# Optimization experiments

Measured on AMD Instinct MI355X. Metric: run time of the kernel, lower is better.

Reference implementation:

```python
import jax, jax.numpy as jnp
import numpy as np

# Hardcoded dims from the source module
B, T, C, H, HS, L, V = 512, 128, 96, 6, 16, 6, 65
FF = 4 * C
EPS = 1e-5  # torch LayerNorm default


def _ln(x, g, b):
    m = jnp.mean(x, axis=-1, keepdims=True)
    v = jnp.mean(jnp.square(x - m), axis=-1, keepdims=True)
    return (x - m) * jax.lax.rsqrt(v + EPS) * g + b


def setup_inputs() -> dict:
    key = jax.random.key(0)
    ks = jax.random.split(key, 24)
    s = 0.02
    n = lambda k, shape: (jax.random.normal(k, shape, dtype=jnp.float32) * s)
    return {
        "idx": jax.random.randint(ks[0], (B, T), 0, V, dtype=jnp.int32),
        "tok_emb": n(ks[1], (V, C)),
        "pos_emb": n(ks[2], (T, C)),
        # per-layer, per-head Q/K/V (each Head has its own bias-free Linear)
        "Wq": n(ks[3], (L, H, C, HS)),
        "Wk": n(ks[4], (L, H, C, HS)),
        "Wv": n(ks[5], (L, H, C, HS)),
        "Wp": n(ks[6], (L, C, C)),
        "bp": jnp.zeros((L, C), jnp.float32),
        "W1": n(ks[7], (L, C, FF)),
        "b1": jnp.zeros((L, FF), jnp.float32),
        "W2": n(ks[8], (L, FF, C)),
        "b2": jnp.zeros((L, C), jnp.float32),
        "ln1_g": jnp.ones((L, C), jnp.float32),
        "ln1_b": jnp.zeros((L, C), jnp.float32),
        "ln2_g": jnp.ones((L, C), jnp.float32),
        "ln2_b": jnp.zeros((L, C), jnp.float32),
        "lnf_g": jnp.ones((C,), jnp.float32),
        "lnf_b": jnp.zeros((C,), jnp.float32),
        "Wlm": n(ks[9], (C, V)),
        "blm": jnp.zeros((V,), jnp.float32),
    }


def _forward(idx, tok_emb, pos_emb, Wq, Wk, Wv, Wp, bp, W1, b1, W2, b2,
             ln1_g, ln1_b, ln2_g, ln2_b, lnf_g, lnf_b, Wlm, blm):
    x = tok_emb[idx] + pos_emb[None, :, :]  # [B,T,C]
    mask = jnp.tril(jnp.ones((T, T), dtype=bool))
    scale = HS ** -0.5

    def block(x, p):
        wq, wk, wv, wp, pb, w1, bb1, w2, bb2, g1, be1, g2, be2 = p
        h = _ln(x, g1, be1)
        q = jnp.einsum('btc,hcd->bhtd', h, wq)
        k = jnp.einsum('btc,hcd->bhtd', h, wk)
        v = jnp.einsum('btc,hcd->bhtd', h, wv)
        w = jnp.einsum('bhtd,bhsd->bhts', q, k) * scale
        w = jnp.where(mask, w, -jnp.inf)
        a = jax.nn.softmax(w, axis=-1)
        o = jnp.einsum('bhts,bhsd->bhtd', a, v)
        o = o.transpose(0, 2, 1, 3).reshape(x.shape[0], T, C)  # concat heads
        x = x + (o @ wp + pb)
        h = _ln(x, g2, be2)
        x = x + (jax.nn.relu(h @ w1 + bb1) @ w2 + bb2)
        return x, None

    params = (Wq, Wk, Wv, Wp, bp, W1, b1, W2, b2, ln1_g, ln1_b, ln2_g, ln2_b)
    x, _ = jax.lax.scan(block, x, params)
    x = _ln(x, lnf_g, lnf_b)
    return x @ Wlm + blm  # logits [B,T,V]


def reference(idx, tok_emb, pos_emb, Wq, Wk, Wv, Wp, bp, W1, b1, W2, b2,
              ln1_g, ln1_b, ln2_g, ln2_b, lnf_g, lnf_b, Wlm, blm):
    return _forward(idx, tok_emb, pos_emb, Wq, Wk, Wv, Wp, bp, W1, b1, W2, b2,
                    ln1_g, ln1_b, ln2_g, ln2_b, lnf_g, lnf_b, Wlm, blm)
```

## Files before the change

kernel.cpp:

```cpp
#include <hip/hip_runtime.h>
#include <hip/hip_bf16.h>

#define BB  512
#define TT  128
#define CC  96
#define HH  6
#define HSZ 16
#define LL  6
#define FFD 384
#define VV  65
#define BT  (BB * TT)

using short8  = __attribute__((ext_vector_type(8))) short;
using short4v = __attribute__((ext_vector_type(4))) short;
using f32x4   = __attribute__((ext_vector_type(4))) float;
using half4   = __attribute__((ext_vector_type(4))) _Float16;

static __device__ __forceinline__ unsigned short f2bf(float f) {
  union { float f; unsigned u; } v{f};
  unsigned r = (v.u + 0x7fff + ((v.u >> 16) & 1)) >> 16;
  return (unsigned short)r;
}
static __device__ __forceinline__ float b2f(unsigned short h) {
  union { unsigned u; float f; } v{(unsigned)h << 16};
  return v.f;
}

__global__ __launch_bounds__(256) void embed_kernel(
    const int* __restrict__ idx, const float* __restrict__ tok,
    const float* __restrict__ pos, float* __restrict__ x) {
  int gid = blockIdx.x * 256 + threadIdx.x;
  int r = gid / 24, c4 = gid % 24;
  int t = r & (TT - 1);
  int token = idx[r];
  const float4 a = *(const float4*)&tok[token * CC + c4 * 4];
  const float4 p = *(const float4*)&pos[t * CC + c4 * 4];
  float4 o;
  o.x = a.x + p.x; o.y = a.y + p.y; o.z = a.z + p.z; o.w = a.w + p.w;
  *(float4*)&x[(size_t)r * CC + c4 * 4] = o;
}

__global__ __launch_bounds__(256) void pack_w(
    const float* __restrict__ Wq, const float* __restrict__ Wk,
    const float* __restrict__ Wv, const float* __restrict__ Wp,
    const float* __restrict__ W1, const float* __restrict__ W2,
    const float* __restrict__ Wlm, unsigned short* __restrict__ out) {
  int job = blockIdx.y;
  int e = blockIdx.x * 256 + threadIdx.x;
  int K, sz; size_t obase;
  if (job < 6)       { K = 96;  sz = 27648; obase = (size_t)job * 27648; }
  else if (job < 12) { K = 96;  sz = 9216;  obase = 165888 + (size_t)(job - 6) * 9216; }
  else if (job < 18) { K = 96;  sz = 36864; obase = 221184 + (size_t)(job - 12) * 36864; }
  else if (job < 24) { K = 384; sz = 36864; obase = 442368 + (size_t)(job - 18) * 36864; }
  else               { K = 96;  sz = 7680;  obase = 663552; }
  if (e >= sz) return;
  int j = e & 7, lane = (e >> 3) & 63, rest = e >> 9;
  int KS = K / 32;
  int ks = rest % KS, cb = rest / KS;
  int k = ks * 32 + (lane >> 4) * 8 + j;
  int n = cb * 16 + (lane & 15);
  float val = 0.f;
  if (job < 6) {
    int src = n / 96, nn = n % 96;
    const float* W = (src == 0) ? Wq : (src == 1) ? Wk : Wv;
    val = W[((size_t)(job * 6 + (nn >> 4)) * 96 + k) * 16 + (nn & 15)];
  } else if (job < 12) {
    val = Wp[(size_t)(job - 6) * 9216 + k * 96 + n];
  } else if (job < 18) {
    val = W1[(size_t)(job - 12) * 36864 + k * 384 + n];
  } else if (job < 24) {
    val = W2[(size_t)(job - 18) * 36864 + k * 96 + n];
  } else {
    if (n < 65) val = Wlm[k * 65 + n];
  }
  out[obase + e] = f2bf(val);
}

template<int K, int N, int NS, bool BIAS, bool RELU, bool RES, bool OUTBF>
__global__ __launch_bounds__(256) void mfma_gemm(
    const unsigned short* __restrict__ A, const unsigned short* __restrict__ Wpk,
    const float* __restrict__ bias, const float* __restrict__ res, void* __restrict__ out) {
  constexpr int KS = K / 32;
  const int lane = threadIdx.x & 63;
  const int wave = threadIdx.x >> 6;
  const int r0 = blockIdx.x * 64 + wave * 16;
  const int c15 = lane & 15, kg = lane >> 4;
  short8 a[KS];
  const unsigned short* ap = A + (size_t)(r0 + c15) * K + kg * 8;
#pragma unroll
  for (int ks = 0; ks < KS; ++ks) a[ks] = *(const short8*)(ap + ks * 32);
  const short8* wf = (const short8*)Wpk;
#pragma unroll 1
  for (int cb = 0; cb < N / 16; ++cb) {
    f32x4 acc = {0.f, 0.f, 0.f, 0.f};
#pragma unroll
    for (int ks = 0; ks < KS; ++ks) {
      short8 b = wf[(cb * KS + ks) * 64 + lane];
      acc = __builtin_amdgcn_mfma_f32_16x16x32_bf16(a[ks], b, acc, 0, 0, 0);
    }
    int n = cb * 16 + c15;
#pragma unroll
    for (int i = 0; i < 4; ++i) {
      int row = r0 + kg * 4 + i;
      if (NS == N || n < NS) {
        float v = acc[i];
        if (BIAS) v += bias[n];
        if (RELU) v = fmaxf(v, 0.f);
        if (RES)  v += res[(size_t)row * NS + n];
        if (OUTBF) ((unsigned short*)out)[(size_t)row * NS + n] = f2bf(v);
        else       ((float*)out)[(size_t)row * NS + n] = v;
      }
    }
  }
}

template<int N, int NS, bool BIAS, bool RELU, bool OUTBF>
__global__ __launch_bounds__(256) void ln_gemm(
    const float* __restrict__ X, const unsigned short* __restrict__ Wpk,
    const float* __restrict__ gamma, const float* __restrict__ beta,
    const float* __restrict__ bias, void* __restrict__ out) {
  const int lane = threadIdx.x & 63;
  const int wave = threadIdx.x >> 6;
  const int r0 = blockIdx.x * 64 + wave * 16;
  const int c15 = lane & 15, kg = lane >> 4;
  const float* xp = X + (size_t)(r0 + c15) * CC + kg * 8;
  float xv[24];
  float s = 0.f, s2 = 0.f;
#pragma unroll
  for (int ks = 0; ks < 3; ++ks) {
    float4 lo = *(const float4*)(xp + ks * 32);
    float4 hi = *(const float4*)(xp + ks * 32 + 4);
    xv[ks * 8 + 0] = lo.x; xv[ks * 8 + 1] = lo.y; xv[ks * 8 + 2] = lo.z; xv[ks * 8 + 3] = lo.w;
    xv[ks * 8 + 4] = hi.x; xv[ks * 8 + 5] = hi.y; xv[ks * 8 + 6] = hi.z; xv[ks * 8 + 7] = hi.w;
  }
#pragma unroll
  for (int i = 0; i < 24; ++i) { s += xv[i]; s2 += xv[i] * xv[i]; }
  s  += __shfl_xor(s, 16);  s  += __shfl_xor(s, 32);
  s2 += __shfl_xor(s2, 16); s2 += __shfl_xor(s2, 32);
  const float mean = s * (1.f / 96.f);
  const float rs = rsqrtf(s2 * (1.f / 96.f) - mean * mean + 1e-5f);
  short8 a[3];
#pragma unroll
  for (int ks = 0; ks < 3; ++ks) {
    const int kb = ks * 32 + kg * 8;
    float4 glo = *(const float4*)&gamma[kb];
    float4 ghi = *(const float4*)&gamma[kb + 4];
    float4 blo = *(const float4*)&beta[kb];
    float4 bhi = *(const float4*)&beta[kb + 4];
    const float gg[8] = {glo.x, glo.y, glo.z, glo.w, ghi.x, ghi.y, ghi.z, ghi.w};
    const float bb[8] = {blo.x, blo.y, blo.z, blo.w, bhi.x, bhi.y, bhi.z, bhi.w};
#pragma unroll
    for (int j = 0; j < 8; ++j)
      a[ks][j] = (short)f2bf((xv[ks * 8 + j] - mean) * rs * gg[j] + bb[j]);
  }
  const short8* wf = (const short8*)Wpk;
#pragma unroll 1
  for (int cb = 0; cb < N / 16; ++cb) {
    f32x4 acc = {0.f, 0.f, 0.f, 0.f};
#pragma unroll
    for (int ks = 0; ks < 3; ++ks) {
      short8 b = wf[(cb * 3 + ks) * 64 + lane];
      acc = __builtin_amdgcn_mfma_f32_16x16x32_bf16(a[ks], b, acc, 0, 0, 0);
    }
    int n = cb * 16 + c15;
#pragma unroll
    for (int i = 0; i < 4; ++i) {
      int row = r0 + kg * 4 + i;
      if (NS == N || n < NS) {
        float v = acc[i];
        if (BIAS) v += bias[n];
        if (RELU) v = fmaxf(v, 0.f);
        if (OUTBF) ((unsigned short*)out)[(size_t)row * NS + n] = f2bf(v);
        else       ((float*)out)[(size_t)row * NS + n] = v;
      }
    }
  }
}

__global__ __launch_bounds__(256) void attn_mfma(
    const unsigned short* __restrict__ qkv, unsigned short* __restrict__ aout) {
  const int b = blockIdx.x / HH, hd = blockIdx.x % HH;
  __shared__ _Float16 Ks[TT][20];
  __shared__ _Float16 Vs[TT][20];
  const size_t base = (size_t)b * TT * 288 + hd * HSZ;
  const int t = threadIdx.x;
  const int r = t >> 1, part = t & 1;

  {
    const short8 k8 = *(const short8*)&qkv[base + (size_t)r * 288 + 96  + part * 8];
    const short8 v8 = *(const short8*)&qkv[base + (size_t)r * 288 + 192 + part * 8];
    half4 klo, khi, vlo, vhi;
#pragma unroll
    for (int j = 0; j < 4; ++j) {
      klo[j] = (_Float16)b2f((unsigned short)k8[j]);
      khi[j] = (_Float16)b2f((unsigned short)k8[4 + j]);
      vlo[j] = (_Float16)b2f((unsigned short)v8[j]);
      vhi[j] = (_Float16)b2f((unsigned short)v8[4 + j]);
    }
    *(half4*)&Ks[r][part * 8]     = klo;
    *(half4*)&Ks[r][part * 8 + 4] = khi;
    *(half4*)&Vs[r][part * 8]     = vlo;
    *(half4*)&Vs[r][part * 8 + 4] = vhi;
  }
  __syncthreads();

  const int lane = t & 63;
  const int w = t >> 6;
  const int q15 = lane & 15, g = lane >> 4;
  const int qt0 = w, qt1 = 7 - w;

  half4 bq[2];
  {
    const short4v qa = *(const short4v*)&qkv[base + (size_t)(qt0 * 16 + q15) * 288 + g * 4];
    const short4v qb = *(const short4v*)&qkv[base + (size_t)(qt1 * 16 + q15) * 288 + g * 4];
#pragma unroll
    for (int j = 0; j < 4; ++j) {
      bq[0][j] = (_Float16)b2f((unsigned short)qa[j]);
      bq[1][j] = (_Float16)b2f((unsigned short)qb[j]);
    }
  }

  half4 ak[8];
#pragma unroll
  for (int kt = 0; kt < 8; ++kt)
    ak[kt] = *(const half4*)&Ks[kt * 16 + q15][g * 4];

  const f32x4 zero = {0.f, 0.f, 0.f, 0.f};
  f32x4 sx[2][8];
#pragma unroll
  for (int kt = 0; kt < 8; ++kt) {
    sx[0][kt] = __builtin_amdgcn_mfma_f32_16x16x16f16(ak[kt], bq[0], zero, 0, 0, 0);
    sx[1][kt] = __builtin_amdgcn_mfma_f32_16x16x16f16(ak[kt], bq[1], zero, 0, 0, 0);
  }

  half4 bp[2][8];
#pragma unroll
  for (int s = 0; s < 2; ++s) {
    const int qt = s ? qt1 : qt0;
    const int qg = qt * 16 + q15;
    float mx = -3.0e38f;
#pragma unroll
    for (int kt = 0; kt < 8; ++kt)
#pragma unroll
      for (int i = 0; i < 4; ++i) {
        int kg = kt * 16 + g * 4 + i;
        float v = (kg <= qg) ? sx[s][kt][i] * 0.25f : -3.0e38f;
        sx[s][kt][i] = v;
        mx = fmaxf(mx, v);
      }
    mx = fmaxf(mx, __shfl_xor(mx, 16));
    mx = fmaxf(mx, __shfl_xor(mx, 32));
    float sum = 0.f;
#pragma unroll
    for (int kt = 0; kt < 8; ++kt)
#pragma unroll
      for (int i = 0; i < 4; ++i) {
        float p = __expf(sx[s][kt][i] - mx);
        sx[s][kt][i] = p;
        sum += p;
      }
    sum += __shfl_xor(sum, 16);
    sum += __shfl_xor(sum, 32);
    float inv = 1.f / sum;
#pragma unroll
    for (int kt = 0; kt < 8; ++kt)
#pragma unroll
      for (int i = 0; i < 4; ++i)
        bp[s][kt][i] = (_Float16)(sx[s][kt][i] * inv);
  }

  f32x4 o0 = zero, o1 = zero;
#pragma unroll
  for (int kt = 0; kt < 8; ++kt) {
    half4 av;
#pragma unroll
    for (int j = 0; j < 4; ++j) av[j] = Vs[kt * 16 + g * 4 + j][q15];
    o0 = __builtin_amdgcn_mfma_f32_16x16x16f16(av, bp[0][kt], o0, 0, 0, 0);
    o1 = __builtin_amdgcn_mfma_f32_16x16x16f16(av, bp[1][kt], o1, 0, 0, 0);
  }

  __syncthreads();
  {
    half4 w0, w1;
#pragma unroll
    for (int i = 0; i < 4; ++i) { w0[i] = (_Float16)o0[i]; w1[i] = (_Float16)o1[i]; }
    *(half4*)&Ks[qt0 * 16 + q15][g * 4] = w0;
    *(half4*)&Ks[qt1 * 16 + q15][g * 4] = w1;
  }
  __syncthreads();
  {
    const half4 a0 = *(const half4*)&Ks[r][part * 8];
    const half4 a1 = *(const half4*)&Ks[r][part * 8 + 4];
    short8 pk;
#pragma unroll
    for (int j = 0; j < 4; ++j) {
      pk[j]     = (short)f2bf((float)a0[j]);
      pk[4 + j] = (short)f2bf((float)a1[j]);
    }
    *(short8*)&aout[(size_t)(b * TT + r) * CC + hd * HSZ + part * 8] = pk;
  }
}

extern "C" void kernel_launch(void* const* d_in, const int* in_sizes, int n_in,
                              void* d_out, int out_size, void* d_ws, size_t ws_size,
                              hipStream_t stream) {
  const int*   idx  = (const int*)d_in[0];
  const float* tok  = (const float*)d_in[1];
  const float* pos  = (const float*)d_in[2];
  const float* Wq   = (const float*)d_in[3];
  const float* Wk   = (const float*)d_in[4];
  const float* Wv   = (const float*)d_in[5];
  const float* Wp   = (const float*)d_in[6];
  const float* bp   = (const float*)d_in[7];
  const float* W1   = (const float*)d_in[8];
  const float* b1   = (const float*)d_in[9];
  const float* W2   = (const float*)d_in[10];
  const float* b2   = (const float*)d_in[11];
  const float* ln1g = (const float*)d_in[12];
  const float* ln1b = (const float*)d_in[13];
  const float* ln2g = (const float*)d_in[14];
  const float* ln2b = (const float*)d_in[15];
  const float* lnfg = (const float*)d_in[16];
  const float* lnfb = (const float*)d_in[17];
  const float* Wlm  = (const float*)d_in[18];
  const float* blm  = (const float*)d_in[19];

  float* x = (float*)d_ws;
  unsigned short* h    = (unsigned short*)(x + (size_t)BT * CC);
  unsigned short* qkvb = h + (size_t)BT * CC;
  unsigned short* ffb  = qkvb;
  unsigned short* wpk  = qkvb + (size_t)BT * FFD;
  const size_t OQKV = 0, OPRJ = 165888, OFF1 = 221184, OFF2 = 442368, OLM = 663552;

  pack_w<<<dim3(144, 25), 256, 0, stream>>>(Wq, Wk, Wv, Wp, W1, W2, Wlm, wpk);
  embed_kernel<<<BT * 24 / 256, 256, 0, stream>>>(idx, tok, pos, x);

  for (int l = 0; l < LL; ++l) {
    ln_gemm<288, 288, false, false, true>
        <<<BT / 64, 256, 0, stream>>>(x, wpk + OQKV + (size_t)l * 27648,
                                      ln1g + l * CC, ln1b + l * CC, nullptr, qkvb);
    attn_mfma<<<BB * HH, 256, 0, stream>>>(qkvb, h);
    mfma_gemm<96, 96, 96, true, false, true, false>
        <<<BT / 64, 256, 0, stream>>>(h, wpk + OPRJ + (size_t)l * 9216, bp + l * CC, x, x);
    ln_gemm<384, 384, true, true, true>
        <<<BT / 64, 256, 0, stream>>>(x, wpk + OFF1 + (size_t)l * 36864,
                                      ln2g + l * CC, ln2b + l * CC, b1 + l * FFD, ffb);
    mfma_gemm<384, 96, 96, true, false, true, false>
        <<<BT / 64, 256, 0, stream>>>(ffb, wpk + OFF2 + (size_t)l * 36864, b2 + l * CC, x, x);
  }

  ln_gemm<80, 65, true, false, false>
      <<<BT / 64, 256, 0, stream>>>(x, wpk + OLM, lnfg, lnfb, blm, (float*)d_out);
}
```

Measured before the change: 742.9 us.

## Fuse LayerNorm, FF1, ReLU and FF2 into one kernel with register-resident intermediates

Measured after the change: 761.3 us. 1.02x slower.

```diff
diff --git a/kernel.cpp b/kernel.cpp
--- a/kernel.cpp
+++ b/kernel.cpp
@@ -24,6 +24,9 @@
 static __device__ __forceinline__ float b2f(unsigned short h) {
   union { unsigned u; float f; } v{(unsigned)h << 16};
   return v.f;
+}
+static __device__ __forceinline__ unsigned short f2h(float f) {
+  union { _Float16 h; unsigned short u; } c; c.h = (_Float16)f; return c.u;
 }
 
 __global__ __launch_bounds__(256) void embed_kernel(
@@ -47,33 +50,43 @@
     const float* __restrict__ Wlm, unsigned short* __restrict__ out) {
   int job = blockIdx.y;
   int e = blockIdx.x * 256 + threadIdx.x;
-  int K, sz; size_t obase;
-  if (job < 6)       { K = 96;  sz = 27648; obase = (size_t)job * 27648; }
-  else if (job < 12) { K = 96;  sz = 9216;  obase = 165888 + (size_t)(job - 6) * 9216; }
-  else if (job < 18) { K = 96;  sz = 36864; obase = 221184 + (size_t)(job - 12) * 36864; }
-  else if (job < 24) { K = 384; sz = 36864; obase = 442368 + (size_t)(job - 18) * 36864; }
-  else               { K = 96;  sz = 7680;  obase = 663552; }
+  int sz; size_t obase;
+  if (job < 6)       { sz = 27648; obase = (size_t)job * 27648; }
+  else if (job < 12) { sz = 9216;  obase = 165888 + (size_t)(job - 6) * 9216; }
+  else if (job < 18) { sz = 36864; obase = 221184 + (size_t)(job - 12) * 36864; }
+  else if (job < 24) { sz = 36864; obase = 442368 + (size_t)(job - 18) * 36864; }
+  else               { sz = 7680;  obase = 663552; }
   if (e >= sz) return;
-  int j = e & 7, lane = (e >> 3) & 63, rest = e >> 9;
-  int KS = K / 32;
-  int ks = rest % KS, cb = rest / KS;
-  int k = ks * 32 + (lane >> 4) * 8 + j;
-  int n = cb * 16 + (lane & 15);
-  float val = 0.f;
-  if (job < 6) {
-    int src = n / 96, nn = n % 96;
-    const float* W = (src == 0) ? Wq : (src == 1) ? Wk : Wv;
-    val = W[((size_t)(job * 6 + (nn >> 4)) * 96 + k) * 16 + (nn & 15)];
-  } else if (job < 12) {
-    val = Wp[(size_t)(job - 6) * 9216 + k * 96 + n];
+
+  if (job < 12 || job >= 24) {
+    int j = e & 7, lane = (e >> 3) & 63, rest = e >> 9;
+    int ks = rest % 3, cb = rest / 3;
+    int k = ks * 32 + (lane >> 4) * 8 + j;
+    int n = cb * 16 + (lane & 15);
+    float val = 0.f;
+    if (job < 6) {
+      int src = n / 96, nn = n % 96;
+      const float* W = (src == 0) ? Wq : (src == 1) ? Wk : Wv;
+      val = W[((size_t)(job * 6 + (nn >> 4)) * 96 + k) * 16 + (nn & 15)];
+    } else if (job < 12) {
+      val = Wp[(size_t)(job - 6) * 9216 + k * 96 + n];
+    } else {
+      if (n < 65) val = Wlm[k * 65 + n];
+    }
+    out[obase + e] = f2bf(val);
   } else if (job < 18) {
-    val = W1[(size_t)(job - 12) * 36864 + k * 384 + n];
-  } else if (job < 24) {
-    val = W2[(size_t)(job - 18) * 36864 + k * 96 + n];
+    int j = e & 3, lane = (e >> 2) & 63, rest = e >> 8;
+    int kt = rest % 6, ft = rest / 6;
+    int k = kt * 16 + (lane >> 4) * 4 + j;
+    int ff = ft * 16 + (lane & 15);
+    out[obase + e] = f2h(W1[(size_t)(job - 12) * 36864 + k * FFD + ff]);
   } else {
-    if (n < 65) val = Wlm[k * 65 + n];
-  }
-  out[obase + e] = f2bf(val);
+    int j = e & 3, lane = (e >> 2) & 63, rest = e >> 8;
+    int kt = rest % 24, ct = rest / 24;
+    int ff = kt * 16 + (lane >> 4) * 4 + j;
+    int c = ct * 16 + (lane & 15);
+    out[obase + e] = f2h(W2[(size_t)(job - 18) * 36864 + ff * CC + c]);
+  }
 }
 
 template<int K, int N, int NS, bool BIAS, bool RELU, bool RES, bool OUTBF>
@@ -174,6 +187,83 @@
         else       ((float*)out)[(size_t)row * NS + n] = v;
       }
     }
+  }
+}
+
+__global__ __launch_bounds__(256) void ff_fused(
+    const float* __restrict__ X, const unsigned short* __restrict__ W1t,
+    const unsigned short* __restrict__ W2t,
+    const float* __restrict__ g2, const float* __restrict__ be2,
+    const float* __restrict__ b1, const float* __restrict__ b2,
+    float* __restrict__ xo) {
+  const int lane = threadIdx.x & 63;
+  const int wave = threadIdx.x >> 6;
+  const int q = lane & 15, g = lane >> 4;
+  const size_t row = (size_t)blockIdx.x * 64 + wave * 16 + q;
+  const float* xp = X + row * CC;
+
+  float xv[24];
+  float s = 0.f, s2 = 0.f;
+#pragma unroll
+  for (int kt = 0; kt < 6; ++kt) {
+    const float4 v = *(const float4*)(xp + kt * 16 + g * 4);
+    xv[kt * 4 + 0] = v.x; xv[kt * 4 + 1] = v.y; xv[kt * 4 + 2] = v.z; xv[kt * 4 + 3] = v.w;
+    s += v.x + v.y + v.z + v.w;
+    s2 += v.x * v.x + v.y * v.y + v.z * v.z + v.w * v.w;
+  }
+  s  += __shfl_xor(s, 16);  s  += __shfl_xor(s, 32);
+  s2 += __shfl_xor(s2, 16); s2 += __shfl_xor(s2, 32);
+  const float mean = s * (1.f / 96.f);
+  const float rs = rsqrtf(s2 * (1.f / 96.f) - mean * mean + 1e-5f);
+
+  half4 bln[6];
+#pragma unroll
+  for (int kt = 0; kt < 6; ++kt) {
+    const float4 gm = *(const float4*)&g2[kt * 16 + g * 4];
+    const float4 bt = *(const float4*)&be2[kt * 16 + g * 4];
+    bln[kt][0] = (_Float16)((xv[kt * 4 + 0] - mean) * rs * gm.x + bt.x);
+    bln[kt][1] = (_Float16)((xv[kt * 4 + 1] - mean) * rs * gm.y + bt.y);
+    bln[kt][2] = (_Float16)((xv[kt * 4 + 2] - mean) * rs * gm.z + bt.z);
+    bln[kt][3] = (_Float16)((xv[kt * 4 + 3] - mean) * rs * gm.w + bt.w);
+  }
+
+  const half4* w1f = (const half4*)W1t;
+  half4 bp1[24];
+  const f32x4 zero = {0.f, 0.f, 0.f, 0.f};
+#pragma unroll
+  for (int ft = 0; ft < 24; ++ft) {
+    f32x4 a1 = zero;
+#pragma unroll
+    for (int kt = 0; kt < 6; ++kt)
+      a1 = __builtin_amdgcn_mfma_f32_16x16x16f16(w1f[(ft * 6 + kt) * 64 + lane], bln[kt], a1, 0, 0, 0);
+    const float4 bb = *(const float4*)&b1[ft * 16 + g * 4];
+    bp1[ft][0] = (_Float16)fmaxf(a1[0] + bb.x, 0.f);
+    bp1[ft][1] = (_Float16)fmaxf(a1[1] + bb.y, 0.f);
+    bp1[ft][2] = (_Float16)fmaxf(a1[2] + bb.z, 0.f);
+    bp1[ft][3] = (_Float16)fmaxf(a1[3] + bb.w, 0.f);
+  }
+
+  const half4* w2f = (const half4*)W2t;
+  f32x4 acc2[6];
+#pragma unroll
+  for (int ct = 0; ct < 6; ++ct) acc2[ct] = zero;
+#pragma unroll
+  for (int kt = 0; kt < 24; ++kt) {
+#pragma unroll
+    for (int ct = 0; ct < 6; ++ct)
+      acc2[ct] = __builtin_amdgcn_mfma_f32_16x16x16f16(w2f[(ct * 24 + kt) * 64 + lane], bp1[kt], acc2[ct], 0, 0, 0);
+  }
+
+  float* op = xo + row * CC;
+#pragma unroll
+  for (int ct = 0; ct < 6; ++ct) {
+    const float4 bb = *(const float4*)&b2[ct * 16 + g * 4];
+    float4 o;
+    o.x = xv[ct * 4 + 0] + acc2[ct][0] + bb.x;
+    o.y = xv[ct * 4 + 1] + acc2[ct][1] + bb.y;
+    o.z = xv[ct * 4 + 2] + acc2[ct][2] + bb.z;
+    o.w = xv[ct * 4 + 3] + acc2[ct][3] + bb.w;
+    *(float4*)(op + ct * 16 + g * 4) = o;
   }
 }
 
@@ -328,7 +418,6 @@
   float* x = (float*)d_ws;
   unsigned short* h    = (unsigned short*)(x + (size_t)BT * CC);
   unsigned short* qkvb = h + (size_t)BT * CC;
-  unsigned short* ffb  = qkvb;
   unsigned short* wpk  = qkvb + (size_t)BT * FFD;
   const size_t OQKV = 0, OPRJ = 165888, OFF1 = 221184, OFF2 = 442368, OLM = 663552;
 
@@ -342,11 +431,10 @@
     attn_mfma<<<BB * HH, 256, 0, stream>>>(qkvb, h);
     mfma_gemm<96, 96, 96, true, false, true, false>
         <<<BT / 64, 256, 0, stream>>>(h, wpk + OPRJ + (size_t)l * 9216, bp + l * CC, x, x);
-    ln_gemm<384, 384, true, true, true>
-        <<<BT / 64, 256, 0, stream>>>(x, wpk + OFF1 + (size_t)l * 36864,
-                                      ln2g + l * CC, ln2b + l * CC, b1 + l * FFD, ffb);
-    mfma_gemm<384, 96, 96, true, false, true, false>
-        <<<BT / 64, 256, 0, stream>>>(ffb, wpk + OFF2 + (size_t)l * 36864, b2 + l * CC, x, x);
+    ff_fused<<<BT / 64, 256, 0, stream>>>(x, wpk + OFF1 + (size_t)l * 36864,
+                                          wpk + OFF2 + (size_t)l * 36864,
+                                          ln2g + l * CC, ln2b + l * CC,
+                                          b1 + l * FFD, b2 + l * CC, x);
   }
 
   ln_gemm<80, 65, true, false, false>
```
